# Optimization experiments

Hardware: AMD Instinct MI355X
Metric: run time of the kernel (lower is better)

The kernel has to match this reference:

```python
import jax, jax.numpy as jnp
import numpy as np

N_NODES = 100000
N_EDGES = 800000
IN_DIM = 128
HIDDEN_DIM = 256
OUT_DIM = 40


def setup_inputs() -> dict:
    key = jax.random.key(0)
    k_x, k_e, k_w1, k_w2 = jax.random.split(key, 4)
    x = jax.random.normal(k_x, (N_NODES, IN_DIM), dtype=jnp.float32)
    edge_index = jax.random.randint(k_e, (2, N_EDGES), 0, N_NODES, dtype=jnp.int32)
    # Glorot-style init like PyG GCNConv
    s1 = 1.0 / np.sqrt(IN_DIM)
    s2 = 1.0 / np.sqrt(HIDDEN_DIM)
    W1 = jax.random.uniform(k_w1, (IN_DIM, HIDDEN_DIM), dtype=jnp.float32, minval=-s1, maxval=s1)
    b1 = jnp.zeros((HIDDEN_DIM,), dtype=jnp.float32)
    W2 = jax.random.uniform(k_w2, (HIDDEN_DIM, OUT_DIM), dtype=jnp.float32, minval=-s2, maxval=s2)
    b2 = jnp.zeros((OUT_DIM,), dtype=jnp.float32)
    return {"x": x, "edge_index": edge_index, "W1": W1, "b1": b1, "W2": W2, "b2": b2}


def _gcn_conv(x, W, b, src, dst, n_nodes):
    # PyG GCNConv: linear transform, add self-loops, symmetric normalization,
    # scatter-add aggregation, then bias.
    h = x @ W  # [N, F_out]
    loops = jnp.arange(n_nodes, dtype=src.dtype)
    s = jnp.concatenate([src, loops])  # [E+N]
    d = jnp.concatenate([dst, loops])
    deg = jax.ops.segment_sum(jnp.ones_like(d, dtype=h.dtype), d, num_segments=n_nodes)
    dinv = jax.lax.rsqrt(jnp.maximum(deg, 1.0))  # deg >= 1 with self-loops
    norm = dinv[s] * dinv[d]  # [E+N]
    msgs = h[s] * norm[:, None]  # [E+N, F_out] -- dominant memory traffic
    out = jax.ops.segment_sum(msgs, d, num_segments=n_nodes)
    return out + b


def reference(x, edge_index, W1, b1, W2, b2):
    src, dst = edge_index[0], edge_index[1]
    n = x.shape[0]
    h = _gcn_conv(x, W1, b1, src, dst, n)
    h = jax.nn.relu(h)
    # dropout is identity in eval mode
    h = _gcn_conv(h, W2, b2, src, dst, n)
    return jax.nn.log_softmax(h, axis=1)
```

## Files before the change

### kernel.cpp

```cpp
#include <hip/hip_runtime.h>
#include <math.h>

#define N_NODES 100000
#define N_EDGES 800000
#define IN_DIM 128
#define HIDDEN_DIM 256
#define OUT_DIM 40
#define CAP 32
#define SHARD_DIV 12500
#define NPAIRS (N_NODES * 64)
#define T1 (HIDDEN_DIM * IN_DIM)
#define T2 (64 * HIDDEN_DIM)

typedef __attribute__((ext_vector_type(8))) __bf16 bf16x8;
typedef __attribute__((ext_vector_type(4))) float f32x4;

#define FIXSC 131072.0f
#define FIXSC_INV 7.62939453125e-6f

__device__ __forceinline__ unsigned short f2bf(float f) {
    unsigned u = __float_as_uint(f);
    unsigned r = (u + 0x7FFFu + ((u >> 16) & 1u)) >> 16;
    return (unsigned short)r;
}
__device__ __forceinline__ float bflo(unsigned v) { return __uint_as_float(v << 16); }
__device__ __forceinline__ float bfhi(unsigned v) { return __uint_as_float(v & 0xFFFF0000u); }

__device__ __forceinline__ bf16x8 ld_frag16(const unsigned short* p) {
    union { uint4 u; bf16x8 b; } t;
    t.u = *(const uint4*)p;
    return t.b;
}

__global__ __launch_bounds__(256) void fill_kernel(const int* __restrict__ src,
                                                   const int* __restrict__ dst,
                                                   int* __restrict__ cnt,
                                                   int* __restrict__ esrc, int e) {
    int shard = blockIdx.x & 7;
    int i = (blockIdx.x >> 3) * 256 + threadIdx.x;
    if (i < e) {
        int d = dst[i];
        if (d / SHARD_DIV == shard) {
            int p = atomicAdd(&cnt[d], 1);
            if (p < CAP) esrc[d * CAP + p] = src[i];
        }
    }
}

__global__ __launch_bounds__(256) void cast_kernel(const float* __restrict__ x,
                                                   const int* __restrict__ cnt,
                                                   unsigned* __restrict__ xs,
                                                   const float* __restrict__ W1,
                                                   unsigned short* __restrict__ W1t,
                                                   const float* __restrict__ W2,
                                                   unsigned short* __restrict__ W2f) {
    int i = blockIdx.x * 256 + threadIdx.x;
    if (i < NPAIRS) {
        float dn = rsqrtf((float)cnt[i >> 6] + 1.0f) * FIXSC;
        float2 v = ((const float2*)x)[i];
        xs[i] = (unsigned)f2bf(v.x * dn) | ((unsigned)f2bf(v.y * dn) << 16);
    }
    if (i < T1) {
        int n = i >> 7, k = i & 127;
        W1t[i] = f2bf(W1[(size_t)k * HIDDEN_DIM + n]);
    } else if (i < T1 + T2) {
        int j = i - T1;
        int e = j & 7, lane = (j >> 3) & 63, frag = j >> 9;
        int l16 = lane & 15, quad = lane >> 4;
        int c2 = frag >> 3, chunk = (frag >> 1) & 3, kk = frag & 1;
        int n = c2 * 16 + l16;
        int k = chunk * 64 + kk * 32 + quad * 8 + e;
        float v = (n < OUT_DIM) ? W2[(size_t)k * OUT_DIM + n] : 0.0f;
        W2f[j] = f2bf(v);
    }
}

__global__ __launch_bounds__(256) void aggx_kernel(const unsigned* __restrict__ xs,
                                                   const int* __restrict__ cnt,
                                                   const int* __restrict__ esrc,
                                                   unsigned* __restrict__ aggxb, int n) {
    int wave = (blockIdx.x * 256 + threadIdx.x) >> 6;
    int lane = threadIdx.x & 63;
    int half = lane >> 5, l32 = lane & 31;
    int node = wave * 2 + half;
    if (node >= n) return;
    int c = cnt[node];
    int m = c < CAP ? c : CAP;
    const uint2* xs2 = (const uint2*)xs;
    uint2 v = xs2[(size_t)node * 32 + l32];
    int ia0 = (int)bflo(v.x), ib0 = (int)bfhi(v.x);
    int ia1 = (int)bflo(v.y), ib1 = (int)bfhi(v.y);
    int base = node * CAP;
    int j = 0;
    for (; j + 7 < m; j += 8) {
        int4 sa = *(const int4*)&esrc[base + j];
        int4 sb = *(const int4*)&esrc[base + j + 4];
        uint2 u0 = xs2[(size_t)sa.x * 32 + l32];
        uint2 u1 = xs2[(size_t)sa.y * 32 + l32];
        uint2 u2 = xs2[(size_t)sa.z * 32 + l32];
        uint2 u3 = xs2[(size_t)sa.w * 32 + l32];
        uint2 u4 = xs2[(size_t)sb.x * 32 + l32];
        uint2 u5 = xs2[(size_t)sb.y * 32 + l32];
        uint2 u6 = xs2[(size_t)sb.z * 32 + l32];
        uint2 u7 = xs2[(size_t)sb.w * 32 + l32];
        ia0 += ((int)bflo(u0.x) + (int)bflo(u1.x)) + ((int)bflo(u2.x) + (int)bflo(u3.x))
             + ((int)bflo(u4.x) + (int)bflo(u5.x)) + ((int)bflo(u6.x) + (int)bflo(u7.x));
        ib0 += ((int)bfhi(u0.x) + (int)bfhi(u1.x)) + ((int)bfhi(u2.x) + (int)bfhi(u3.x))
             + ((int)bfhi(u4.x) + (int)bfhi(u5.x)) + ((int)bfhi(u6.x) + (int)bfhi(u7.x));
        ia1 += ((int)bflo(u0.y) + (int)bflo(u1.y)) + ((int)bflo(u2.y) + (int)bflo(u3.y))
             + ((int)bflo(u4.y) + (int)bflo(u5.y)) + ((int)bflo(u6.y) + (int)bflo(u7.y));
        ib1 += ((int)bfhi(u0.y) + (int)bfhi(u1.y)) + ((int)bfhi(u2.y) + (int)bfhi(u3.y))
             + ((int)bfhi(u4.y) + (int)bfhi(u5.y)) + ((int)bfhi(u6.y) + (int)bfhi(u7.y));
    }
    for (; j + 3 < m; j += 4) {
        int4 s = *(const int4*)&esrc[base + j];
        uint2 u0 = xs2[(size_t)s.x * 32 + l32];
        uint2 u1 = xs2[(size_t)s.y * 32 + l32];
        uint2 u2 = xs2[(size_t)s.z * 32 + l32];
        uint2 u3 = xs2[(size_t)s.w * 32 + l32];
        ia0 += ((int)bflo(u0.x) + (int)bflo(u1.x)) + ((int)bflo(u2.x) + (int)bflo(u3.x));
        ib0 += ((int)bfhi(u0.x) + (int)bfhi(u1.x)) + ((int)bfhi(u2.x) + (int)bfhi(u3.x));
        ia1 += ((int)bflo(u0.y) + (int)bflo(u1.y)) + ((int)bflo(u2.y) + (int)bflo(u3.y));
        ib1 += ((int)bfhi(u0.y) + (int)bfhi(u1.y)) + ((int)bfhi(u2.y) + (int)bfhi(u3.y));
    }
    for (; j < m; j++) {
        uint2 u = xs2[(size_t)esrc[base + j] * 32 + l32];
        ia0 += (int)bflo(u.x); ib0 += (int)bfhi(u.x);
        ia1 += (int)bflo(u.y); ib1 += (int)bfhi(u.y);
    }
    float k = rsqrtf((float)c + 1.0f) * FIXSC_INV;
    uint2 o;
    o.x = (unsigned)f2bf((float)ia0 * k) | ((unsigned)f2bf((float)ib0 * k) << 16);
    o.y = (unsigned)f2bf((float)ia1 * k) | ((unsigned)f2bf((float)ib1 * k) << 16);
    ((uint2*)aggxb)[(size_t)node * 32 + l32] = o;
}

#define BSTR 136
#define HSTR 72
__device__ __forceinline__ void phase2_epi(f32x4 (&acc)[16], int rowg,
                                           unsigned short* hw,
                                           const unsigned short* __restrict__ W2f,
                                           const float* __restrict__ b1,
                                           const int* __restrict__ cnt,
                                           unsigned short* __restrict__ h2s,
                                           int lane, int quad, int l16, int M) {
    f32x4 acc2[3];
#pragma unroll
    for (int c2 = 0; c2 < 3; c2++) acc2[c2] = (f32x4){0.f, 0.f, 0.f, 0.f};
#pragma unroll
    for (int chunk = 0; chunk < 4; chunk++) {
#pragma unroll
        for (int cc = 0; cc < 4; cc++) {
            int ct = chunk * 4 + cc;
            float bb = b1[ct * 16 + l16];
#pragma unroll
            for (int r = 0; r < 4; r++) {
                int row = quad * 4 + r;
                float v = fmaxf(acc[ct][r] + bb, 0.0f);
                hw[row * HSTR + cc * 16 + l16] = f2bf(v);
            }
        }
#pragma unroll
        for (int kk = 0; kk < 2; kk++) {
            bf16x8 af2 = ld_frag16(&hw[l16 * HSTR + kk * 32 + quad * 8]);
#pragma unroll
            for (int c2 = 0; c2 < 3; c2++) {
                bf16x8 bfr = ld_frag16(&W2f[(size_t)((c2 * 8 + chunk * 2 + kk) * 64 + lane) * 8]);
                acc2[c2] = __builtin_amdgcn_mfma_f32_16x16x32_bf16(af2, bfr, acc2[c2], 0, 0, 0);
            }
        }
    }
#pragma unroll
    for (int c2 = 0; c2 < 3; c2++) {
        int col = c2 * 16 + l16;
#pragma unroll
        for (int r = 0; r < 4; r++) {
            int gm = rowg + quad * 4 + r;
            if (gm < M) {
                float v = acc2[c2][r] * (rsqrtf((float)cnt[gm] + 1.0f) * FIXSC);
                h2s[(size_t)gm * 64 + col] = f2bf(v);
            }
        }
    }
}

__global__ __launch_bounds__(256, 2) void gemm12_kernel(const unsigned short* __restrict__ A,
                                                        const unsigned short* __restrict__ W1t,
                                                        const unsigned short* __restrict__ W2f,
                                                        const float* __restrict__ b1,
                                                        const int* __restrict__ cnt,
                                                        unsigned short* __restrict__ h2s,
                                                        int M) {
    __shared__ __align__(16) unsigned short Bs[256 * BSTR];
    __shared__ __align__(16) unsigned short Hs[4 * 16 * HSTR];
    int tid = threadIdx.x;
    int wv = tid >> 6, lane = tid & 63;
    int quad = lane >> 4, l16 = lane & 15;
    int row0 = blockIdx.x * 128 + wv * 32;

#pragma unroll
    for (int rep = 0; rep < 16; rep++) {
        int lin = rep * 256 + tid;
        int row = lin >> 4, ch = lin & 15;
        *(uint4*)&Bs[row * BSTR + ch * 8] = *(const uint4*)&W1t[(size_t)row * 128 + ch * 8];
    }

    f32x4 zero4 = {0.f, 0.f, 0.f, 0.f};
    f32x4 accA[16], accB[16];
#pragma unroll
    for (int ct = 0; ct < 16; ct++) { accA[ct] = zero4; accB[ct] = zero4; }

    __syncthreads();

#pragma unroll
    for (int k0 = 0; k0 < 128; k0 += 32) {
        int gmA = row0 + l16, gmB = row0 + 16 + l16;
        union { uint4 u; bf16x8 b; } cvA, cvB;
        cvA.u = make_uint4(0u, 0u, 0u, 0u);
        cvB.u = make_uint4(0u, 0u, 0u, 0u);
        if (gmA < M) cvA.u = *(const uint4*)&A[(size_t)gmA * 128 + k0 + quad * 8];
        if (gmB < M) cvB.u = *(const uint4*)&A[(size_t)gmB * 128 + k0 + quad * 8];
#pragma unroll
        for (int ct = 0; ct < 16; ct++) {
            bf16x8 bfr = ld_frag16(&Bs[(ct * 16 + l16) * BSTR + k0 + quad * 8]);
            accA[ct] = __builtin_amdgcn_mfma_f32_16x16x32_bf16(cvA.b, bfr, accA[ct], 0, 0, 0);
            accB[ct] = __builtin_amdgcn_mfma_f32_16x16x32_bf16(cvB.b, bfr, accB[ct], 0, 0, 0);
        }
    }

    unsigned short* hw = &Hs[wv * 16 * HSTR];
    phase2_epi(accA, row0,      hw, W2f, b1, cnt, h2s, lane, quad, l16, M);
    phase2_epi(accB, row0 + 16, hw, W2f, b1, cnt, h2s, lane, quad, l16, M);
}

__global__ __launch_bounds__(256) void agg2_kernel(const unsigned* __restrict__ h2u,
                                                   const int* __restrict__ cnt,
                                                   const int* __restrict__ esrc,
                                                   const float* __restrict__ b2,
                                                   float* __restrict__ out, int n) {
    int wave = (blockIdx.x * 256 + threadIdx.x) >> 6;
    int lane = threadIdx.x & 63;
    int half = lane >> 5, l32 = lane & 31;
    int node = wave * 2 + half;
    if (node >= n) return;
    int c = cnt[node];
    int m = c < CAP ? c : CAP;
    int base = node * CAP;
    unsigned v = h2u[(size_t)node * 32 + l32];
    int ia = (int)bflo(v), ib = (int)bfhi(v);
    int j = 0;
    for (; j + 7 < m; j += 8) {
        int s0 = esrc[base + j],     s1 = esrc[base + j + 1];
        int s2 = esrc[base + j + 2], s3 = esrc[base + j + 3];
        int s4 = esrc[base + j + 4], s5 = esrc[base + j + 5];
        int s6 = esrc[base + j + 6], s7 = esrc[base + j + 7];
        unsigned u0 = h2u[(size_t)s0 * 32 + l32];
        unsigned u1 = h2u[(size_t)s1 * 32 + l32];
        unsigned u2 = h2u[(size_t)s2 * 32 + l32];
        unsigned u3 = h2u[(size_t)s3 * 32 + l32];
        unsigned u4 = h2u[(size_t)s4 * 32 + l32];
        unsigned u5 = h2u[(size_t)s5 * 32 + l32];
        unsigned u6 = h2u[(size_t)s6 * 32 + l32];
        unsigned u7 = h2u[(size_t)s7 * 32 + l32];
        ia += ((int)bflo(u0) + (int)bflo(u1)) + ((int)bflo(u2) + (int)bflo(u3))
            + ((int)bflo(u4) + (int)bflo(u5)) + ((int)bflo(u6) + (int)bflo(u7));
        ib += ((int)bfhi(u0) + (int)bfhi(u1)) + ((int)bfhi(u2) + (int)bfhi(u3))
            + ((int)bfhi(u4) + (int)bfhi(u5)) + ((int)bfhi(u6) + (int)bfhi(u7));
    }
    for (; j + 3 < m; j += 4) {
        int s0 = esrc[base + j],     s1 = esrc[base + j + 1];
        int s2 = esrc[base + j + 2], s3 = esrc[base + j + 3];
        unsigned u0 = h2u[(size_t)s0 * 32 + l32];
        unsigned u1 = h2u[(size_t)s1 * 32 + l32];
        unsigned u2 = h2u[(size_t)s2 * 32 + l32];
        unsigned u3 = h2u[(size_t)s3 * 32 + l32];
        ia += ((int)bflo(u0) + (int)bflo(u1)) + ((int)bflo(u2) + (int)bflo(u3));
        ib += ((int)bfhi(u0) + (int)bfhi(u1)) + ((int)bfhi(u2) + (int)bfhi(u3));
    }
    for (; j < m; j++) {
        unsigned u = h2u[(size_t)esrc[base + j] * 32 + l32];
        ia += (int)bflo(u); ib += (int)bfhi(u);
    }
    float k = rsqrtf((float)c + 1.0f) * FIXSC_INV;
    int f0 = 2 * l32;
    bool a0 = (f0 < OUT_DIM), a1 = (f0 + 1 < OUT_DIM);
    float v0 = a0 ? fmaf((float)ia, k, b2[f0]) : -INFINITY;
    float v1 = a1 ? fmaf((float)ib, k, b2[f0 + 1]) : -INFINITY;
    float mx = fmaxf(v0, v1);
#pragma unroll
    for (int o = 16; o > 0; o >>= 1) mx = fmaxf(mx, __shfl_xor(mx, o));
    float e = (a0 ? __expf(v0 - mx) : 0.0f) + (a1 ? __expf(v1 - mx) : 0.0f);
#pragma unroll
    for (int o = 16; o > 0; o >>= 1) e += __shfl_xor(e, o);
    if (a0) {
        float ls = __logf(e);
        *(float2*)&out[(size_t)node * OUT_DIM + f0] = make_float2(v0 - mx - ls, v1 - mx - ls);
    }
}

extern "C" void kernel_launch(void* const* d_in, const int* in_sizes, int n_in,
                              void* d_out, int out_size, void* d_ws, size_t ws_size,
                              hipStream_t stream) {
    const float* x  = (const float*)d_in[0];
    const int* ei   = (const int*)d_in[1];
    const float* W1 = (const float*)d_in[2];
    const float* b1 = (const float*)d_in[3];
    const float* W2 = (const float*)d_in[4];
    const float* b2 = (const float*)d_in[5];
    float* out = (float*)d_out;

    const int* src = ei;
    const int* dst = ei + N_EDGES;

    char* ws = (char*)d_ws;
    size_t off = 0;
    auto carve = [&](size_t bytes) -> char* {
        char* p = ws + off;
        off = (off + bytes + 255) & ~(size_t)255;
        return p;
    };
    int*      cnt   = (int*)     carve((size_t)N_NODES * 4);
    int*      esrc  = (int*)     carve((size_t)N_NODES * CAP * 4);
    unsigned* xs    = (unsigned*)carve((size_t)N_NODES * 64 * 4);
    unsigned short* W1t = (unsigned short*)carve((size_t)T1 * 2);
    unsigned short* W2f = (unsigned short*)carve((size_t)T2 * 2);
    unsigned* aggxb = (unsigned*)carve((size_t)N_NODES * 64 * 4);
    unsigned short* h2s = (unsigned short*)carve((size_t)N_NODES * 64 * 2);

    hipMemsetAsync(cnt, 0, (size_t)N_NODES * 4, stream);
    fill_kernel<<<((N_EDGES + 255) / 256) * 8, 256, 0, stream>>>(src, dst, cnt, esrc, N_EDGES);
    cast_kernel<<<(NPAIRS + 255) / 256, 256, 0, stream>>>(x, cnt, xs, W1, W1t, W2, W2f);
    aggx_kernel<<<((N_NODES + 1) / 2 * 64 + 255) / 256, 256, 0, stream>>>(
        xs, cnt, esrc, aggxb, N_NODES);
    gemm12_kernel<<<(N_NODES + 127) / 128, 256, 0, stream>>>(
        (const unsigned short*)aggxb, W1t, W2f, b1, cnt, h2s, N_NODES);
    agg2_kernel<<<((N_NODES + 1) / 2 * 64 + 255) / 256, 256, 0, stream>>>(
        (const unsigned*)h2s, cnt, esrc, b2, out, N_NODES);
}
```

Measured before the change: 244.5 us.

## Fuse first-layer neighbor gather into GEMM kernel via swizzled LDS A-tile

```diff
diff --git a/kernel.cpp b/kernel.cpp
--- a/kernel.cpp
+++ b/kernel.cpp
@@ -75,18 +75,12 @@
     }
 }
 
-__global__ __launch_bounds__(256) void aggx_kernel(const unsigned* __restrict__ xs,
-                                                   const int* __restrict__ cnt,
-                                                   const int* __restrict__ esrc,
-                                                   unsigned* __restrict__ aggxb, int n) {
-    int wave = (blockIdx.x * 256 + threadIdx.x) >> 6;
-    int lane = threadIdx.x & 63;
-    int half = lane >> 5, l32 = lane & 31;
-    int node = wave * 2 + half;
-    if (node >= n) return;
+__device__ __forceinline__ uint2 gather_node(const uint2* __restrict__ xs2,
+                                             const int* __restrict__ cnt,
+                                             const int* __restrict__ esrc,
+                                             int node, int l32) {
     int c = cnt[node];
     int m = c < CAP ? c : CAP;
-    const uint2* xs2 = (const uint2*)xs;
     uint2 v = xs2[(size_t)node * 32 + l32];
     int ia0 = (int)bflo(v.x), ib0 = (int)bfhi(v.x);
     int ia1 = (int)bflo(v.y), ib1 = (int)bfhi(v.y);
@@ -132,10 +126,9 @@
     uint2 o;
     o.x = (unsigned)f2bf((float)ia0 * k) | ((unsigned)f2bf((float)ib0 * k) << 16);
     o.y = (unsigned)f2bf((float)ia1 * k) | ((unsigned)f2bf((float)ib1 * k) << 16);
-    ((uint2*)aggxb)[(size_t)node * 32 + l32] = o;
-}
-
-#define BSTR 136
+    return o;
+}
+
 #define HSTR 72
 __device__ __forceinline__ void phase2_epi(f32x4 (&acc)[16], int rowg,
                                            unsigned short* hw,
@@ -184,25 +177,29 @@
     }
 }
 
-__global__ __launch_bounds__(256, 2) void gemm12_kernel(const unsigned short* __restrict__ A,
+__global__ __launch_bounds__(256, 2) void gemm12_kernel(const unsigned* __restrict__ xs,
+                                                        const int* __restrict__ cnt,
+                                                        const int* __restrict__ esrc,
                                                         const unsigned short* __restrict__ W1t,
                                                         const unsigned short* __restrict__ W2f,
                                                         const float* __restrict__ b1,
-                                                        const int* __restrict__ cnt,
                                                         unsigned short* __restrict__ h2s,
                                                         int M) {
-    __shared__ __align__(16) unsigned short Bs[256 * BSTR];
+    __shared__ __align__(16) unsigned short As[128 * 128];
     __shared__ __align__(16) unsigned short Hs[4 * 16 * HSTR];
     int tid = threadIdx.x;
     int wv = tid >> 6, lane = tid & 63;
     int quad = lane >> 4, l16 = lane & 15;
+    int half = lane >> 5, l32 = lane & 31;
     int row0 = blockIdx.x * 128 + wv * 32;
 
-#pragma unroll
-    for (int rep = 0; rep < 16; rep++) {
-        int lin = rep * 256 + tid;
-        int row = lin >> 4, ch = lin & 15;
-        *(uint4*)&Bs[row * BSTR + ch * 8] = *(const uint4*)&W1t[(size_t)row * 128 + ch * 8];
+    const uint2* xs2 = (const uint2*)xs;
+    for (int it = 0; it < 16; it++) {
+        int lrow = wv * 32 + it * 2 + half;
+        int node = blockIdx.x * 128 + lrow;
+        uint2 o = make_uint2(0u, 0u);
+        if (node < M) o = gather_node(xs2, cnt, esrc, node, l32);
+        *(uint2*)&As[lrow * 128 + ((l32 * 4) ^ ((lrow & 7) << 3))] = o;
     }
 
     f32x4 zero4 = {0.f, 0.f, 0.f, 0.f};
@@ -214,17 +211,14 @@
 
 #pragma unroll
     for (int k0 = 0; k0 < 128; k0 += 32) {
-        int gmA = row0 + l16, gmB = row0 + 16 + l16;
-        union { uint4 u; bf16x8 b; } cvA, cvB;
-        cvA.u = make_uint4(0u, 0u, 0u, 0u);
-        cvB.u = make_uint4(0u, 0u, 0u, 0u);
-        if (gmA < M) cvA.u = *(const uint4*)&A[(size_t)gmA * 128 + k0 + quad * 8];
-        if (gmB < M) cvB.u = *(const uint4*)&A[(size_t)gmB * 128 + k0 + quad * 8];
+        int rA = wv * 32 + l16, rB = wv * 32 + 16 + l16;
+        bf16x8 afA = ld_frag16(&As[rA * 128 + ((k0 + quad * 8) ^ ((rA & 7) << 3))]);
+        bf16x8 afB = ld_frag16(&As[rB * 128 + ((k0 + quad * 8) ^ ((rB & 7) << 3))]);
 #pragma unroll
         for (int ct = 0; ct < 16; ct++) {
-            bf16x8 bfr = ld_frag16(&Bs[(ct * 16 + l16) * BSTR + k0 + quad * 8]);
-            accA[ct] = __builtin_amdgcn_mfma_f32_16x16x32_bf16(cvA.b, bfr, accA[ct], 0, 0, 0);
-            accB[ct] = __builtin_amdgcn_mfma_f32_16x16x32_bf16(cvB.b, bfr, accB[ct], 0, 0, 0);
+            bf16x8 bfr = ld_frag16(&W1t[(size_t)(ct * 16 + l16) * 128 + k0 + quad * 8]);
+            accA[ct] = __builtin_amdgcn_mfma_f32_16x16x32_bf16(afA, bfr, accA[ct], 0, 0, 0);
+            accB[ct] = __builtin_amdgcn_mfma_f32_16x16x32_bf16(afB, bfr, accB[ct], 0, 0, 0);
         }
     }
 
@@ -324,16 +318,13 @@
     unsigned* xs    = (unsigned*)carve((size_t)N_NODES * 64 * 4);
     unsigned short* W1t = (unsigned short*)carve((size_t)T1 * 2);
     unsigned short* W2f = (unsigned short*)carve((size_t)T2 * 2);
-    unsigned* aggxb = (unsigned*)carve((size_t)N_NODES * 64 * 4);
     unsigned short* h2s = (unsigned short*)carve((size_t)N_NODES * 64 * 2);
 
     hipMemsetAsync(cnt, 0, (size_t)N_NODES * 4, stream);
     fill_kernel<<<((N_EDGES + 255) / 256) * 8, 256, 0, stream>>>(src, dst, cnt, esrc, N_EDGES);
     cast_kernel<<<(NPAIRS + 255) / 256, 256, 0, stream>>>(x, cnt, xs, W1, W1t, W2, W2f);
-    aggx_kernel<<<((N_NODES + 1) / 2 * 64 + 255) / 256, 256, 0, stream>>>(
-        xs, cnt, esrc, aggxb, N_NODES);
     gemm12_kernel<<<(N_NODES + 127) / 128, 256, 0, stream>>>(
-        (const unsigned short*)aggxb, W1t, W2f, b1, cnt, h2s, N_NODES);
+        xs, cnt, esrc, W1t, W2f, b1, h2s, N_NODES);
     agg2_kernel<<<((N_NODES + 1) / 2 * 64 + 255) / 256, 256, 0, stream>>>(
         (const unsigned*)h2s, cnt, esrc, b2, out, N_NODES);
 }
```

Measured after the change: 325.8 us. +33.3%, slower.

## Fuse edge fill and input cast into one kernel, defer degree scaling to aggregation

Applied to the files above, without the earlier changes.

```diff
diff --git a/kernel.cpp b/kernel.cpp
--- a/kernel.cpp
+++ b/kernel.cpp
@@ -11,6 +11,8 @@
 #define NPAIRS (N_NODES * 64)
 #define T1 (HIDDEN_DIM * IN_DIM)
 #define T2 (64 * HIDDEN_DIM)
+#define FILL_BLKS (((N_EDGES + 1023) / 1024) * 8)
+#define CAST_BLKS ((NPAIRS + 255) / 256)
 
 typedef __attribute__((ext_vector_type(8))) __bf16 bf16x8;
 typedef __attribute__((ext_vector_type(4))) float f32x4;
@@ -32,46 +34,69 @@
     return t.b;
 }
 
-__global__ __launch_bounds__(256) void fill_kernel(const int* __restrict__ src,
-                                                   const int* __restrict__ dst,
-                                                   int* __restrict__ cnt,
-                                                   int* __restrict__ esrc, int e) {
-    int shard = blockIdx.x & 7;
-    int i = (blockIdx.x >> 3) * 256 + threadIdx.x;
-    if (i < e) {
-        int d = dst[i];
-        if (d / SHARD_DIV == shard) {
-            int p = atomicAdd(&cnt[d], 1);
-            if (p < CAP) esrc[d * CAP + p] = src[i];
-        }
-    }
-}
-
-__global__ __launch_bounds__(256) void cast_kernel(const float* __restrict__ x,
-                                                   const int* __restrict__ cnt,
-                                                   unsigned* __restrict__ xs,
-                                                   const float* __restrict__ W1,
-                                                   unsigned short* __restrict__ W1t,
-                                                   const float* __restrict__ W2,
-                                                   unsigned short* __restrict__ W2f) {
-    int i = blockIdx.x * 256 + threadIdx.x;
-    if (i < NPAIRS) {
-        float dn = rsqrtf((float)cnt[i >> 6] + 1.0f) * FIXSC;
-        float2 v = ((const float2*)x)[i];
-        xs[i] = (unsigned)f2bf(v.x * dn) | ((unsigned)f2bf(v.y * dn) << 16);
-    }
-    if (i < T1) {
-        int n = i >> 7, k = i & 127;
-        W1t[i] = f2bf(W1[(size_t)k * HIDDEN_DIM + n]);
-    } else if (i < T1 + T2) {
-        int j = i - T1;
-        int e = j & 7, lane = (j >> 3) & 63, frag = j >> 9;
-        int l16 = lane & 15, quad = lane >> 4;
-        int c2 = frag >> 3, chunk = (frag >> 1) & 3, kk = frag & 1;
-        int n = c2 * 16 + l16;
-        int k = chunk * 64 + kk * 32 + quad * 8 + e;
-        float v = (n < OUT_DIM) ? W2[(size_t)k * OUT_DIM + n] : 0.0f;
-        W2f[j] = f2bf(v);
+__global__ __launch_bounds__(256) void fillcast_kernel(const int* __restrict__ src,
+                                                       const int* __restrict__ dst,
+                                                       int* __restrict__ cnt,
+                                                       int* __restrict__ esrc,
+                                                       const float* __restrict__ x,
+                                                       unsigned* __restrict__ xs,
+                                                       const float* __restrict__ W1,
+                                                       unsigned short* __restrict__ W1t,
+                                                       const float* __restrict__ W2,
+                                                       unsigned short* __restrict__ W2f) {
+    int bid = blockIdx.x;
+    if (bid < FILL_BLKS) {
+        int shard = bid & 7;
+        int i0 = (bid >> 3) * 1024 + threadIdx.x * 4;
+        if (i0 + 3 < N_EDGES) {
+            int4 d4 = *(const int4*)&dst[i0];
+            if (d4.x / SHARD_DIV == shard) {
+                int p = atomicAdd(&cnt[d4.x], 1);
+                if (p < CAP) esrc[d4.x * CAP + p] = src[i0];
+            }
+            if (d4.y / SHARD_DIV == shard) {
+                int p = atomicAdd(&cnt[d4.y], 1);
+                if (p < CAP) esrc[d4.y * CAP + p] = src[i0 + 1];
+            }
+            if (d4.z / SHARD_DIV == shard) {
+                int p = atomicAdd(&cnt[d4.z], 1);
+                if (p < CAP) esrc[d4.z * CAP + p] = src[i0 + 2];
+            }
+            if (d4.w / SHARD_DIV == shard) {
+                int p = atomicAdd(&cnt[d4.w], 1);
+                if (p < CAP) esrc[d4.w * CAP + p] = src[i0 + 3];
+            }
+        } else {
+            for (int j = 0; j < 4; j++) {
+                int i = i0 + j;
+                if (i < N_EDGES) {
+                    int d = dst[i];
+                    if (d / SHARD_DIV == shard) {
+                        int p = atomicAdd(&cnt[d], 1);
+                        if (p < CAP) esrc[d * CAP + p] = src[i];
+                    }
+                }
+            }
+        }
+    } else {
+        int i = (bid - FILL_BLKS) * 256 + threadIdx.x;
+        if (i < NPAIRS) {
+            float2 v = ((const float2*)x)[i];
+            xs[i] = (unsigned)f2bf(v.x * FIXSC) | ((unsigned)f2bf(v.y * FIXSC) << 16);
+        }
+        if (i < T1) {
+            int n = i >> 7, k = i & 127;
+            W1t[i] = f2bf(W1[(size_t)k * HIDDEN_DIM + n]);
+        } else if (i < T1 + T2) {
+            int j = i - T1;
+            int e = j & 7, lane = (j >> 3) & 63, frag = j >> 9;
+            int l16 = lane & 15, quad = lane >> 4;
+            int c2 = frag >> 3, chunk = (frag >> 1) & 3, kk = frag & 1;
+            int n = c2 * 16 + l16;
+            int k = chunk * 64 + kk * 32 + quad * 8 + e;
+            float v = (n < OUT_DIM) ? W2[(size_t)k * OUT_DIM + n] : 0.0f;
+            W2f[j] = f2bf(v);
+        }
     }
 }
 
@@ -87,14 +112,23 @@
     int c = cnt[node];
     int m = c < CAP ? c : CAP;
     const uint2* xs2 = (const uint2*)xs;
+    float dn = rsqrtf((float)c + 1.0f);
     uint2 v = xs2[(size_t)node * 32 + l32];
-    int ia0 = (int)bflo(v.x), ib0 = (int)bfhi(v.x);
-    int ia1 = (int)bflo(v.y), ib1 = (int)bfhi(v.y);
+    int ia0 = (int)(bflo(v.x) * dn), ib0 = (int)(bfhi(v.x) * dn);
+    int ia1 = (int)(bflo(v.y) * dn), ib1 = (int)(bfhi(v.y) * dn);
     int base = node * CAP;
     int j = 0;
     for (; j + 7 < m; j += 8) {
         int4 sa = *(const int4*)&esrc[base + j];
         int4 sb = *(const int4*)&esrc[base + j + 4];
+        float d0 = rsqrtf((float)cnt[sa.x] + 1.0f);
+        float d1 = rsqrtf((float)cnt[sa.y] + 1.0f);
+        float d2 = rsqrtf((float)cnt[sa.z] + 1.0f);
+        float d3 = rsqrtf((float)cnt[sa.w] + 1.0f);
+        float d4 = rsqrtf((float)cnt[sb.x] + 1.0f);
+        float d5 = rsqrtf((float)cnt[sb.y] + 1.0f);
+        float d6 = rsqrtf((float)cnt[sb.z] + 1.0f);
+        float d7 = rsqrtf((float)cnt[sb.w] + 1.0f);
         uint2 u0 = xs2[(size_t)sa.x * 32 + l32];
         uint2 u1 = xs2[(size_t)sa.y * 32 + l32];
         uint2 u2 = xs2[(size_t)sa.z * 32 + l32];
@@ -103,32 +137,38 @@
         uint2 u5 = xs2[(size_t)sb.y * 32 + l32];
         uint2 u6 = xs2[(size_t)sb.z * 32 + l32];
         uint2 u7 = xs2[(size_t)sb.w * 32 + l32];
-        ia0 += ((int)bflo(u0.x) + (int)bflo(u1.x)) + ((int)bflo(u2.x) + (int)bflo(u3.x))
-             + ((int)bflo(u4.x) + (int)bflo(u5.x)) + ((int)bflo(u6.x) + (int)bflo(u7.x));
-        ib0 += ((int)bfhi(u0.x) + (int)bfhi(u1.x)) + ((int)bfhi(u2.x) + (int)bfhi(u3.x))
-             + ((int)bfhi(u4.x) + (int)bfhi(u5.x)) + ((int)bfhi(u6.x) + (int)bfhi(u7.x));
-        ia1 += ((int)bflo(u0.y) + (int)bflo(u1.y)) + ((int)bflo(u2.y) + (int)bflo(u3.y))
-             + ((int)bflo(u4.y) + (int)bflo(u5.y)) + ((int)bflo(u6.y) + (int)bflo(u7.y));
-        ib1 += ((int)bfhi(u0.y) + (int)bfhi(u1.y)) + ((int)bfhi(u2.y) + (int)bfhi(u3.y))
-             + ((int)bfhi(u4.y) + (int)bfhi(u5.y)) + ((int)bfhi(u6.y) + (int)bfhi(u7.y));
+        ia0 += ((int)(bflo(u0.x) * d0) + (int)(bflo(u1.x) * d1)) + ((int)(bflo(u2.x) * d2) + (int)(bflo(u3.x) * d3))
+             + ((int)(bflo(u4.x) * d4) + (int)(bflo(u5.x) * d5)) + ((int)(bflo(u6.x) * d6) + (int)(bflo(u7.x) * d7));
+        ib0 += ((int)(bfhi(u0.x) * d0) + (int)(bfhi(u1.x) * d1)) + ((int)(bfhi(u2.x) * d2) + (int)(bfhi(u3.x) * d3))
+             + ((int)(bfhi(u4.x) * d4) + (int)(bfhi(u5.x) * d5)) + ((int)(bfhi(u6.x) * d6) + (int)(bfhi(u7.x) * d7));
+        ia1 += ((int)(bflo(u0.y) * d0) + (int)(bflo(u1.y) * d1)) + ((int)(bflo(u2.y) * d2) + (int)(bflo(u3.y) * d3))
+             + ((int)(bflo(u4.y) * d4) + (int)(bflo(u5.y) * d5)) + ((int)(bflo(u6.y) * d6) + (int)(bflo(u7.y) * d7));
+        ib1 += ((int)(bfhi(u0.y) * d0) + (int)(bfhi(u1.y) * d1)) + ((int)(bfhi(u2.y) * d2) + (int)(bfhi(u3.y) * d3))
+             + ((int)(bfhi(u4.y) * d4) + (int)(bfhi(u5.y) * d5)) + ((int)(bfhi(u6.y) * d6) + (int)(bfhi(u7.y) * d7));
     }
     for (; j + 3 < m; j += 4) {
         int4 s = *(const int4*)&esrc[base + j];
+        float d0 = rsqrtf((float)cnt[s.x] + 1.0f);
+        float d1 = rsqrtf((float)cnt[s.y] + 1.0f);
+        float d2 = rsqrtf((float)cnt[s.z] + 1.0f);
+        float d3 = rsqrtf((float)cnt[s.w] + 1.0f);
         uint2 u0 = xs2[(size_t)s.x * 32 + l32];
         uint2 u1 = xs2[(size_t)s.y * 32 + l32];
         uint2 u2 = xs2[(size_t)s.z * 32 + l32];
         uint2 u3 = xs2[(size_t)s.w * 32 + l32];
-        ia0 += ((int)bflo(u0.x) + (int)bflo(u1.x)) + ((int)bflo(u2.x) + (int)bflo(u3.x));
-        ib0 += ((int)bfhi(u0.x) + (int)bfhi(u1.x)) + ((int)bfhi(u2.x) + (int)bfhi(u3.x));
-        ia1 += ((int)bflo(u0.y) + (int)bflo(u1.y)) + ((int)bflo(u2.y) + (int)bflo(u3.y));
-        ib1 += ((int)bfhi(u0.y) + (int)bfhi(u1.y)) + ((int)bfhi(u2.y) + (int)bfhi(u3.y));
+        ia0 += ((int)(bflo(u0.x) * d0) + (int)(bflo(u1.x) * d1)) + ((int)(bflo(u2.x) * d2) + (int)(bflo(u3.x) * d3));
+        ib0 += ((int)(bfhi(u0.x) * d0) + (int)(bfhi(u1.x) * d1)) + ((int)(bfhi(u2.x) * d2) + (int)(bfhi(u3.x) * d3));
+        ia1 += ((int)(bflo(u0.y) * d0) + (int)(bflo(u1.y) * d1)) + ((int)(bflo(u2.y) * d2) + (int)(bflo(u3.y) * d3));
+        ib1 += ((int)(bfhi(u0.y) * d0) + (int)(bfhi(u1.y) * d1)) + ((int)(bfhi(u2.y) * d2) + (int)(bfhi(u3.y) * d3));
     }
     for (; j < m; j++) {
-        uint2 u = xs2[(size_t)esrc[base + j] * 32 + l32];
-        ia0 += (int)bflo(u.x); ib0 += (int)bfhi(u.x);
-        ia1 += (int)bflo(u.y); ib1 += (int)bfhi(u.y);
-    }
-    float k = rsqrtf((float)c + 1.0f) * FIXSC_INV;
+        int s = esrc[base + j];
+        float d = rsqrtf((float)cnt[s] + 1.0f);
+        uint2 u = xs2[(size_t)s * 32 + l32];
+        ia0 += (int)(bflo(u.x) * d); ib0 += (int)(bfhi(u.x) * d);
+        ia1 += (int)(bflo(u.y) * d); ib1 += (int)(bfhi(u.y) * d);
+    }
+    float k = dn * FIXSC_INV;
     uint2 o;
     o.x = (unsigned)f2bf((float)ia0 * k) | ((unsigned)f2bf((float)ib0 * k) << 16);
     o.y = (unsigned)f2bf((float)ia1 * k) | ((unsigned)f2bf((float)ib1 * k) << 16);
@@ -328,8 +368,8 @@
     unsigned short* h2s = (unsigned short*)carve((size_t)N_NODES * 64 * 2);
 
     hipMemsetAsync(cnt, 0, (size_t)N_NODES * 4, stream);
-    fill_kernel<<<((N_EDGES + 255) / 256) * 8, 256, 0, stream>>>(src, dst, cnt, esrc, N_EDGES);
-    cast_kernel<<<(NPAIRS + 255) / 256, 256, 0, stream>>>(x, cnt, xs, W1, W1t, W2, W2f);
+    fillcast_kernel<<<FILL_BLKS + CAST_BLKS, 256, 0, stream>>>(
+        src, dst, cnt, esrc, x, xs, W1, W1t, W2, W2f);
     aggx_kernel<<<((N_NODES + 1) / 2 * 64 + 255) / 256, 256, 0, stream>>>(
         xs, cnt, esrc, aggxb, N_NODES);
     gemm12_kernel<<<(N_NODES + 127) / 128, 256, 0, stream>>>(
```

Result: no change. 244.1 us (-0.2%).
